# Optimization experiments

Measured on AMD Instinct MI355X. Metric: run time of the kernel, lower is better.

Reference implementation:

```python
import jax, jax.numpy as jnp
import numpy as np

B, S, D, H = 2, 2048, 1024, 16
HD = D // H            # head_dim = 64
CHUNK = 1024           # hard-coded in the torch module
ROPE_THETA = 10000.0


def setup_inputs() -> dict:
    key = jax.random.key(0)
    ks = jax.random.split(key, 5)
    hidden_states = jax.random.normal(ks[0], (B, S, D), dtype=jnp.float32)
    # Precomputed RoPE frequencies: freqs_cis[s, j] = exp(i * s * theta_j),
    # stored as real [S, HD//2, 2] = (cos, sin).
    inv_freq = 1.0 / (ROPE_THETA ** (np.arange(0, HD, 2, dtype=np.float32) / HD))
    ang = np.outer(np.arange(S, dtype=np.float32), inv_freq)  # [S, HD//2]
    freqs_cis = jnp.stack([jnp.cos(ang), jnp.sin(ang)], axis=-1).astype(jnp.float32)
    scale = 0.02
    Wq = jax.random.normal(ks[1], (D, D), dtype=jnp.float32) * scale
    Wk = jax.random.normal(ks[2], (D, D), dtype=jnp.float32) * scale
    Wv = jax.random.normal(ks[3], (D, D), dtype=jnp.float32) * scale
    Wo = jax.random.normal(ks[4], (D, D), dtype=jnp.float32) * scale
    return {"hidden_states": hidden_states, "freqs_cis": freqs_cis,
            "Wq": Wq, "Wk": Wk, "Wv": Wv, "Wo": Wo}


def _apply_rope(x, freqs_cis):
    # x: [B, S, H, HD]; freqs_cis: [S, HD//2, 2] (cos, sin)
    b, s, h, hd = x.shape
    xr = x.reshape(b, s, h, hd // 2, 2)
    a, bb = xr[..., 0], xr[..., 1]
    c = freqs_cis[:s, :, 0][None, :, None, :]  # broadcast over batch, heads
    d = freqs_cis[:s, :, 1][None, :, None, :]
    # complex multiply (a + ib)(c + id)
    out = jnp.stack([a * c - bb * d, a * d + bb * c], axis=-1)
    return out.reshape(b, s, h, hd)


def reference(hidden_states, freqs_cis, Wq, Wk, Wv, Wo):
    b, s, dm = hidden_states.shape
    q = (hidden_states @ Wq).reshape(b, s, H, HD)
    k = (hidden_states @ Wk).reshape(b, s, H, HD)
    v = (hidden_states @ Wv).reshape(b, s, H, HD)
    q = _apply_rope(q, freqs_cis)
    k = _apply_rope(k, freqs_cis)
    q = q.transpose(0, 2, 1, 3)  # [B, H, S, HD]
    k = k.transpose(0, 2, 1, 3)
    v = v.transpose(0, 2, 1, 3)
    scaling = HD ** (-0.5)
    out = jnp.zeros_like(q)
    # Faithful replication of the (buggy) chunked attention: softmax is
    # normalized PER key-chunk, then chunk outputs are summed.
    for i in range(0, s, CHUNK):
        j = min(i + CHUNK, s)
        w = jnp.einsum('bhqd,bhkd->bhqk', q, k[:, :, i:j]) * scaling
        w = jax.nn.softmax(w.astype(jnp.float32), axis=-1).astype(q.dtype)
        out = out + jnp.einsum('bhqk,bhkd->bhqd', w, v[:, :, i:j])
    out = out.transpose(0, 2, 1, 3).reshape(b, s, dm)
    return out @ Wo
```

## Files before the change

kernel.cpp:

```cpp
#include <hip/hip_runtime.h>
#include <hip/hip_bf16.h>
#include <cstdint>

typedef __bf16 bf16x8 __attribute__((ext_vector_type(8)));
typedef float f32x4 __attribute__((ext_vector_type(4)));
typedef float f32x16 __attribute__((ext_vector_type(16)));

#define MFMA16(a, b, c) __builtin_amdgcn_mfma_f32_16x16x32_bf16(a, b, c, 0, 0, 0)
#define MFMA32(a, b, c) __builtin_amdgcn_mfma_f32_32x32x16_bf16(a, b, c, 0, 0, 0)

__device__ __forceinline__ void gload_lds16(const void* g, void* l) {
  __builtin_amdgcn_global_load_lds(
      (const __attribute__((address_space(1))) unsigned int*)g,
      (__attribute__((address_space(3))) unsigned int*)l, 16, 0, 0);
}

__device__ __forceinline__ unsigned short f2bf(float x) {
  union { float f; uint32_t u; } v; v.f = x;
  uint32_t r = v.u + 0x7fff + ((v.u >> 16) & 1);
  return (unsigned short)(r >> 16);
}
__device__ __forceinline__ float bf2f(unsigned short h) {
  union { float f; uint32_t u; } v; v.u = ((uint32_t)h) << 16;
  return v.f;
}
__device__ __forceinline__ f32x16 fzero16() {
  f32x16 v;
#pragma unroll
  for (int i = 0; i < 16; ++i) v[i] = 0.f;
  return v;
}

__device__ __forceinline__ void ptrans(const f32x16& sv, float& rsum,
                                       bf16x8& f0, bf16x8& f1) {
  float ps[16];
#pragma unroll
  for (int r = 0; r < 16; ++r) ps[r] = __builtin_exp2f(sv[r]);
  float rs = 0.f;
#pragma unroll
  for (int r = 0; r < 16; ++r) rs += ps[r];
  rsum += rs;
  bf16x8 a, b;
#pragma unroll
  for (int r = 0; r < 8; ++r) a[r] = (__bf16)ps[r];
#pragma unroll
  for (int r = 0; r < 8; ++r) b[r] = (__bf16)ps[8 + r];
  f0 = a; f1 = b;
}

__global__ __launch_bounds__(256) void k_split(const float* __restrict__ x,
                                               unsigned short* __restrict__ hi, int n4) {
  int i = blockIdx.x * blockDim.x + threadIdx.x;
  if (i >= n4) return;
  float4 v = ((const float4*)x)[i];
  ushort4 h;
  h.x = f2bf(v.x); h.y = f2bf(v.y); h.z = f2bf(v.z); h.w = f2bf(v.w);
  ((ushort4*)hi)[i] = h;
}

__global__ __launch_bounds__(256) void k_wsplit(
    const float* __restrict__ Wq, const float* __restrict__ Wk,
    const float* __restrict__ Wv, const float* __restrict__ Wo,
    unsigned short* __restrict__ WtqH, unsigned short* __restrict__ WtkH,
    unsigned short* __restrict__ WtvH, unsigned short* __restrict__ WtoH) {
  const int z = blockIdx.z;
  const float* W = (z == 0) ? Wq : (z == 1) ? Wk : (z == 2) ? Wv : Wo;
  unsigned short* WtH = (z == 0) ? WtqH : (z == 1) ? WtkH : (z == 2) ? WtvH : WtoH;
  __shared__ float tile[32][33];
  const int bx = blockIdx.x, by = blockIdx.y;
  const int tx = threadIdx.x & 31, ty = threadIdx.x >> 5;
#pragma unroll
  for (int i = 0; i < 4; ++i)
    tile[ty + i * 8][tx] = W[(size_t)(by * 32 + ty + i * 8) * 1024 + bx * 32 + tx];
  __syncthreads();
#pragma unroll
  for (int i = 0; i < 4; ++i) {
    float v = tile[tx][ty + i * 8];
    WtH[(size_t)(bx * 32 + ty + i * 8) * 1024 + by * 32 + tx] = f2bf(v);
  }
}

__global__ __launch_bounds__(256, 2) void k_qkv(
    const unsigned short* __restrict__ hsH,
    const unsigned short* __restrict__ WqH, const unsigned short* __restrict__ WkH,
    const unsigned short* __restrict__ WvH, const float* __restrict__ freqs,
    unsigned short* __restrict__ qB, unsigned short* __restrict__ kB,
    unsigned short* __restrict__ vB) {
  __shared__ unsigned short Ah[128 * 32], Bh[128 * 32];
  const int tid = threadIdx.x;
  const int bm = blockIdx.y, bn = blockIdx.x;
  const int w = bn >> 3;
  const int n0 = (bn & 7) * 128;
  const unsigned short* WH = (w == 0) ? WqH : (w == 1) ? WkH : WvH;
  const int lane = tid & 63, wave = tid >> 6;
  const int wm = (wave & 1) * 64, wn = (wave >> 1) * 64;
  const int l15 = lane & 15, lq = lane >> 4;

  f32x4 acc[4][4];
#pragma unroll
  for (int i = 0; i < 4; i++)
#pragma unroll
    for (int j = 0; j < 4; j++) acc[i][j] = (f32x4){0.f, 0.f, 0.f, 0.f};

  const char* baseA = (const char*)hsH + (size_t)(bm * 128) * 2048;
  const char* baseB = (const char*)WH + (size_t)n0 * 2048;
  const int off0 = tid << 4, row0 = off0 >> 6, seg0 = off0 & 63;
  const int off1 = (tid + 256) << 4, row1 = off1 >> 6, seg1 = off1 & 63;

  for (int k0 = 0; k0 < 1024; k0 += 32) {
    __syncthreads();
    gload_lds16(baseA + (size_t)row0 * 2048 + k0 * 2 + seg0, (char*)Ah + wave * 1024);
    gload_lds16(baseB + (size_t)row0 * 2048 + k0 * 2 + seg0, (char*)Bh + wave * 1024);
    gload_lds16(baseA + (size_t)row1 * 2048 + k0 * 2 + seg1,
                (char*)Ah + 4096 + wave * 1024);
    gload_lds16(baseB + (size_t)row1 * 2048 + k0 * 2 + seg1,
                (char*)Bh + 4096 + wave * 1024);
    __syncthreads();
    bf16x8 ah[4], bh[4];
#pragma unroll
    for (int i = 0; i < 4; ++i) {
      ah[i] = *(const bf16x8*)&Ah[(wm + i * 16 + l15) * 32 + lq * 8];
      bh[i] = *(const bf16x8*)&Bh[(wn + i * 16 + l15) * 32 + lq * 8];
    }
#pragma unroll
    for (int i = 0; i < 4; ++i)
#pragma unroll
      for (int j = 0; j < 4; ++j) acc[i][j] = MFMA16(ah[i], bh[j], acc[i][j]);
  }

  unsigned short* dst = (w == 0) ? qB : (w == 1) ? kB : vB;
#pragma unroll
  for (int i = 0; i < 4; ++i) {
#pragma unroll
    for (int j = 0; j < 4; ++j) {
      int colw = n0 + wn + j * 16 + l15;
      int h = colw >> 6, d = colw & 63;
#pragma unroll
      for (int r = 0; r < 4; ++r) {
        int rowg = bm * 128 + wm + i * 16 + lq * 4 + r;
        int s = rowg & 2047, b = rowg >> 11;
        float val = acc[i][j][r];
        size_t bhb = (size_t)(b * 16 + h) * 131072;
        if (w < 2) {
          float partner = __shfl_xor(val, 1);
          int jj = d >> 1;
          float2 cssn = ((const float2*)freqs)[s * 32 + jj];
          float cs = cssn.x, sn = cssn.y;
          float res = (d & 1) ? (partner * sn + val * cs) : (val * cs - partner * sn);
          if (w == 0) {
            res *= 0.18033688011112042f;
            dst[(((size_t)(b * 16 + h)) * 2048 + s) * 64 + d] = f2bf(res);
          } else {
            size_t off = (size_t)(s >> 10) * 65536 + ((s >> 6) & 15) * 4096 +
                         ((s >> 5) & 1) * 2048 + (d >> 4) * 512 +
                         ((s & 31) + 32 * ((d >> 3) & 1)) * 8 + (d & 7);
            dst[bhb + off] = f2bf(res);
          }
        } else {
          int sp = (s & ~12) | ((s & 4) << 1) | ((s & 8) >> 1);
          size_t off = (size_t)(sp >> 10) * 65536 + ((sp >> 6) & 15) * 4096 +
                       (d >> 5) * 2048 + ((sp >> 4) & 3) * 512 +
                       ((d & 31) + 32 * ((sp >> 3) & 1)) * 8 + (sp & 7);
          dst[bhb + off] = f2bf(val);
        }
      }
    }
  }
}

__global__ __launch_bounds__(256, 4) void k_attn(
    const unsigned short* __restrict__ qB, const unsigned short* __restrict__ kB,
    const unsigned short* __restrict__ vB,
    unsigned short* __restrict__ c0, unsigned short* __restrict__ c1) {
  __shared__ unsigned short KV[2][8192];
  const int tid = threadIdx.x, lane = tid & 63, wave = tid >> 6;
  const int l31 = lane & 31, lh = lane >> 5;
  const int bid = blockIdx.x;
  const int x = (bid >> 3) & 15;
  const int gg = (bid & 7) + 8 * (bid >> 7);
  const int bh = gg & 31;
  const int chunk = gg >> 5;
  const int q0 = x * 128 + wave * 32;
  const size_t base = (size_t)bh * 131072;

  bf16x8 qf[4];
#pragma unroll
  for (int ks = 0; ks < 4; ++ks)
    qf[ks] = *(const bf16x8*)(qB + base + (size_t)(q0 + l31) * 64 + ks * 16 + lh * 8);

  const unsigned short* kblk = kB + base + chunk * 65536;
  const unsigned short* vblk = vB + base + chunk * 65536;

  gload_lds16((const char*)kblk + tid * 16, (char*)KV[0] + wave * 1024);
  gload_lds16((const char*)kblk + 4096 + tid * 16, (char*)KV[0] + 4096 + wave * 1024);
  gload_lds16((const char*)vblk + tid * 16, (char*)KV[0] + 8192 + wave * 1024);
  gload_lds16((const char*)vblk + 4096 + tid * 16, (char*)KV[0] + 12288 + wave * 1024);
  __syncthreads();

  f32x16 o[2];
#pragma unroll
  for (int a = 0; a < 2; ++a) o[a] = fzero16();
  float rsum = 0.f;

  for (int kb = 0; kb < 16; ++kb) {
    const unsigned short* Kc = KV[kb & 1];
    const unsigned short* Vc = KV[kb & 1] + 4096;
    if (kb < 15) {
      const char* ks_ = (const char*)(kblk + (kb + 1) * 4096);
      const char* vs_ = (const char*)(vblk + (kb + 1) * 4096);
      char* db = (char*)KV[(kb + 1) & 1];
      gload_lds16(ks_ + tid * 16, db + wave * 1024);
      gload_lds16(ks_ + 4096 + tid * 16, db + 4096 + wave * 1024);
      gload_lds16(vs_ + tid * 16, db + 8192 + wave * 1024);
      gload_lds16(vs_ + 4096 + tid * 16, db + 12288 + wave * 1024);
    }

    f32x16 sA = fzero16(), sB = fzero16();
    {
      bf16x8 kf[4];
#pragma unroll
      for (int ks = 0; ks < 4; ++ks)
        kf[ks] = *(const bf16x8*)(Kc + ks * 512 + lane * 8);
      __builtin_amdgcn_s_setprio(1);
#pragma unroll
      for (int ks = 0; ks < 4; ++ks) sA = MFMA32(kf[ks], qf[ks], sA);
      __builtin_amdgcn_s_setprio(0);
    }
    {
      bf16x8 kf[4];
#pragma unroll
      for (int ks = 0; ks < 4; ++ks)
        kf[ks] = *(const bf16x8*)(Kc + 2048 + ks * 512 + lane * 8);
      __builtin_amdgcn_s_setprio(1);
#pragma unroll
      for (int ks = 0; ks < 4; ++ks) sB = MFMA32(kf[ks], qf[ks], sB);
      __builtin_amdgcn_s_setprio(0);
    }

    bf16x8 vf[2][4];
#pragma unroll
    for (int dt = 0; dt < 2; ++dt)
#pragma unroll
      for (int ks = 0; ks < 4; ++ks)
        vf[dt][ks] = *(const bf16x8*)(Vc + dt * 2048 + ks * 512 + lane * 8);

    bf16x8 fA0, fA1, fB0, fB1;
    ptrans(sA, rsum, fA0, fA1);
    __builtin_amdgcn_s_setprio(1);
    o[0] = MFMA32(vf[0][0], fA0, o[0]);
    o[1] = MFMA32(vf[1][0], fA0, o[1]);
    o[0] = MFMA32(vf[0][1], fA1, o[0]);
    o[1] = MFMA32(vf[1][1], fA1, o[1]);
    __builtin_amdgcn_s_setprio(0);
    ptrans(sB, rsum, fB0, fB1);
    __builtin_amdgcn_s_setprio(1);
    o[0] = MFMA32(vf[0][2], fB0, o[0]);
    o[1] = MFMA32(vf[1][2], fB0, o[1]);
    o[0] = MFMA32(vf[0][3], fB1, o[0]);
    o[1] = MFMA32(vf[1][3], fB1, o[1]);
    __builtin_amdgcn_s_setprio(0);

    __syncthreads();
  }

  unsigned short* cB = chunk ? c1 : c0;
  const int b = bh >> 4, h = bh & 15;
  float lsum = rsum + __shfl_xor(rsum, 32);
  float inv = 1.f / lsum;
  int s = q0 + l31;
#pragma unroll
  for (int dt = 0; dt < 2; ++dt)
#pragma unroll
    for (int g = 0; g < 4; ++g) {
      int d = dt * 32 + 4 * lh + 8 * g;
      size_t idx = ((size_t)(b * 2048 + s)) * 1024 + h * 64 + d;
      ushort4 hv;
#pragma unroll
      for (int t = 0; t < 4; ++t)
        ((unsigned short*)&hv)[t] = f2bf(o[dt][g * 4 + t] * inv);
      *(ushort4*)(cB + idx) = hv;
    }
}

__global__ __launch_bounds__(256) void k_comb(const unsigned short* __restrict__ c0,
                                              const unsigned short* __restrict__ c1,
                                              unsigned short* __restrict__ outB,
                                              int n8) {
  int i = blockIdx.x * blockDim.x + threadIdx.x;
  if (i >= n8) return;
  uint4 a = ((const uint4*)c0)[i];
  uint4 b = ((const uint4*)c1)[i];
  uint4 r;
  const unsigned short* pa = (const unsigned short*)&a;
  const unsigned short* pb = (const unsigned short*)&b;
  unsigned short* pr = (unsigned short*)&r;
#pragma unroll
  for (int j = 0; j < 8; ++j) pr[j] = f2bf(bf2f(pa[j]) + bf2f(pb[j]));
  ((uint4*)outB)[i] = r;
}

__global__ __launch_bounds__(256, 2) void k_out(const unsigned short* __restrict__ A,
                                                const unsigned short* __restrict__ B,
                                                float* __restrict__ out) {
  __shared__ unsigned short Ah[128 * 32], Bh[64 * 32];
  const int tid = threadIdx.x;
  const int bm = blockIdx.y, n0 = blockIdx.x * 64;
  const int lane = tid & 63, wave = tid >> 6;
  const int wm = (wave & 1) * 64, wn = (wave >> 1) * 32;
  const int l15 = lane & 15, lq = lane >> 4;

  f32x4 acc[4][2];
#pragma unroll
  for (int i = 0; i < 4; i++)
#pragma unroll
    for (int j = 0; j < 2; j++) acc[i][j] = (f32x4){0.f, 0.f, 0.f, 0.f};

  const char* baseA = (const char*)A + (size_t)(bm * 128) * 2048;
  const char* baseB = (const char*)B + (size_t)n0 * 2048;
  const int off0 = tid << 4, row0 = off0 >> 6, seg0 = off0 & 63;
  const int off1 = (tid + 256) << 4, row1 = off1 >> 6, seg1 = off1 & 63;

  for (int k0 = 0; k0 < 1024; k0 += 32) {
    __syncthreads();
    gload_lds16(baseA + (size_t)row0 * 2048 + k0 * 2 + seg0, (char*)Ah + wave * 1024);
    gload_lds16(baseA + (size_t)row1 * 2048 + k0 * 2 + seg1,
                (char*)Ah + 4096 + wave * 1024);
    gload_lds16(baseB + (size_t)row0 * 2048 + k0 * 2 + seg0, (char*)Bh + wave * 1024);
    __syncthreads();
    bf16x8 ah[4], bh[2];
#pragma unroll
    for (int i = 0; i < 4; ++i)
      ah[i] = *(const bf16x8*)&Ah[(wm + i * 16 + l15) * 32 + lq * 8];
#pragma unroll
    for (int j = 0; j < 2; ++j)
      bh[j] = *(const bf16x8*)&Bh[(wn + j * 16 + l15) * 32 + lq * 8];
#pragma unroll
    for (int i = 0; i < 4; ++i)
#pragma unroll
      for (int j = 0; j < 2; ++j) acc[i][j] = MFMA16(ah[i], bh[j], acc[i][j]);
  }
#pragma unroll
  for (int i = 0; i < 4; ++i)
#pragma unroll
    for (int j = 0; j < 2; ++j) {
      int colw = n0 + wn + j * 16 + l15;
#pragma unroll
      for (int r = 0; r < 4; ++r) {
        int rowg = bm * 128 + wm + i * 16 + lq * 4 + r;
        out[(size_t)rowg * 1024 + colw] = acc[i][j][r];
      }
    }
}

extern "C" void kernel_launch(void* const* d_in, const int* in_sizes, int n_in,
                              void* d_out, int out_size, void* d_ws, size_t ws_size,
                              hipStream_t stream) {
  const float* hs = (const float*)d_in[0];
  const float* freqs = (const float*)d_in[1];
  const float* Wq = (const float*)d_in[2];
  const float* Wk = (const float*)d_in[3];
  const float* Wv = (const float*)d_in[4];
  const float* Wo = (const float*)d_in[5];
  float* out = (float*)d_out;

  const size_t MD = (size_t)4096 * 1024;
  const size_t WW = (size_t)1024 * 1024;
  unsigned short* hsH = (unsigned short*)d_ws;
  unsigned short* WtqH = hsH + MD;
  unsigned short* WtkH = WtqH + WW;
  unsigned short* WtvH = WtkH + WW;
  unsigned short* WtoH = WtvH + WW;
  unsigned short* qB = WtoH + WW;
  unsigned short* kB = qB + MD;
  unsigned short* vB = kB + MD;
  unsigned short* c0 = vB + MD;
  unsigned short* c1 = c0 + MD;
  unsigned short* attnB = hsH;

  k_split<<<4096, 256, 0, stream>>>(hs, hsH, (int)(MD / 4));
  k_wsplit<<<dim3(32, 32, 4), 256, 0, stream>>>(Wq, Wk, Wv, Wo,
                                                WtqH, WtkH, WtvH, WtoH);
  k_qkv<<<dim3(24, 32), 256, 0, stream>>>(hsH, WtqH, WtkH, WtvH, freqs, qB, kB, vB);
  k_attn<<<1024, 256, 0, stream>>>(qB, kB, vB, c0, c1);
  k_comb<<<2048, 256, 0, stream>>>(c0, c1, attnB, (int)(MD / 8));
  k_out<<<dim3(16, 32), 256, 0, stream>>>(attnB, WtoH, out);
}
```

Before: 213.2 us.

## Fuse hidden-state bf16 conversion into QKV GEMM and merge attention chunks

```diff
diff --git a/kernel.cpp b/kernel.cpp
--- a/kernel.cpp
+++ b/kernel.cpp
@@ -20,10 +20,6 @@
   uint32_t r = v.u + 0x7fff + ((v.u >> 16) & 1);
   return (unsigned short)(r >> 16);
 }
-__device__ __forceinline__ float bf2f(unsigned short h) {
-  union { float f; uint32_t u; } v; v.u = ((uint32_t)h) << 16;
-  return v.f;
-}
 __device__ __forceinline__ f32x16 fzero16() {
   f32x16 v;
 #pragma unroll
@@ -46,16 +42,6 @@
 #pragma unroll
   for (int r = 0; r < 8; ++r) b[r] = (__bf16)ps[8 + r];
   f0 = a; f1 = b;
-}
-
-__global__ __launch_bounds__(256) void k_split(const float* __restrict__ x,
-                                               unsigned short* __restrict__ hi, int n4) {
-  int i = blockIdx.x * blockDim.x + threadIdx.x;
-  if (i >= n4) return;
-  float4 v = ((const float4*)x)[i];
-  ushort4 h;
-  h.x = f2bf(v.x); h.y = f2bf(v.y); h.z = f2bf(v.z); h.w = f2bf(v.w);
-  ((ushort4*)hi)[i] = h;
 }
 
 __global__ __launch_bounds__(256) void k_wsplit(
@@ -81,12 +67,13 @@
 }
 
 __global__ __launch_bounds__(256, 2) void k_qkv(
-    const unsigned short* __restrict__ hsH,
+    const float* __restrict__ hs,
     const unsigned short* __restrict__ WqH, const unsigned short* __restrict__ WkH,
     const unsigned short* __restrict__ WvH, const float* __restrict__ freqs,
     unsigned short* __restrict__ qB, unsigned short* __restrict__ kB,
     unsigned short* __restrict__ vB) {
-  __shared__ unsigned short Ah[128 * 32], Bh[128 * 32];
+  __shared__ float Af[128 * 32];
+  __shared__ unsigned short Bh[128 * 32];
   const int tid = threadIdx.x;
   const int bm = blockIdx.y, bn = blockIdx.x;
   const int w = bn >> 3;
@@ -102,24 +89,38 @@
 #pragma unroll
     for (int j = 0; j < 4; j++) acc[i][j] = (f32x4){0.f, 0.f, 0.f, 0.f};
 
-  const char* baseA = (const char*)hsH + (size_t)(bm * 128) * 2048;
+  const char* baseA = (const char*)hs + (size_t)(bm * 128) * 4096;
   const char* baseB = (const char*)WH + (size_t)n0 * 2048;
-  const int off0 = tid << 4, row0 = off0 >> 6, seg0 = off0 & 63;
-  const int off1 = (tid + 256) << 4, row1 = off1 >> 6, seg1 = off1 & 63;
+  const int off0 = tid << 4, brow0 = off0 >> 6, bseg0 = off0 & 63;
+  const int off1 = (tid + 256) << 4, brow1 = off1 >> 6, bseg1 = off1 & 63;
 
   for (int k0 = 0; k0 < 1024; k0 += 32) {
     __syncthreads();
-    gload_lds16(baseA + (size_t)row0 * 2048 + k0 * 2 + seg0, (char*)Ah + wave * 1024);
-    gload_lds16(baseB + (size_t)row0 * 2048 + k0 * 2 + seg0, (char*)Bh + wave * 1024);
-    gload_lds16(baseA + (size_t)row1 * 2048 + k0 * 2 + seg1,
-                (char*)Ah + 4096 + wave * 1024);
-    gload_lds16(baseB + (size_t)row1 * 2048 + k0 * 2 + seg1,
+#pragma unroll
+    for (int g = 0; g < 4; ++g) {
+      int offa = g * 4096 + tid * 16;
+      int arow = offa >> 7, aseg = offa & 127;
+      gload_lds16(baseA + (size_t)arow * 4096 + k0 * 4 + aseg,
+                  (char*)Af + g * 4096 + wave * 1024);
+    }
+    gload_lds16(baseB + (size_t)brow0 * 2048 + k0 * 2 + bseg0,
+                (char*)Bh + wave * 1024);
+    gload_lds16(baseB + (size_t)brow1 * 2048 + k0 * 2 + bseg1,
                 (char*)Bh + 4096 + wave * 1024);
     __syncthreads();
     bf16x8 ah[4], bh[4];
 #pragma unroll
     for (int i = 0; i < 4; ++i) {
-      ah[i] = *(const bf16x8*)&Ah[(wm + i * 16 + l15) * 32 + lq * 8];
+      int ar = wm + i * 16 + l15;
+      f32x4 a0 = *(const f32x4*)&Af[ar * 32 + lq * 8];
+      f32x4 a1 = *(const f32x4*)&Af[ar * 32 + lq * 8 + 4];
+      bf16x8 v;
+#pragma unroll
+      for (int j = 0; j < 4; ++j) {
+        v[j] = (__bf16)a0[j];
+        v[4 + j] = (__bf16)a1[j];
+      }
+      ah[i] = v;
       bh[i] = *(const bf16x8*)&Bh[(wn + i * 16 + l15) * 32 + lq * 8];
     }
 #pragma unroll
@@ -168,18 +169,70 @@
   }
 }
 
-__global__ __launch_bounds__(256, 4) void k_attn(
+#define ATTN_KB(KB, OAC, RS, PREF)                                            \
+  {                                                                           \
+    const unsigned short* Kc = KV[(KB) & 1];                                  \
+    const unsigned short* Vc = KV[(KB) & 1] + 4096;                           \
+    if (PREF) {                                                               \
+      const char* ks_ = (const char*)(kblk + ((KB) + 1) * 4096);              \
+      const char* vs_ = (const char*)(vblk + ((KB) + 1) * 4096);              \
+      char* db = (char*)KV[((KB) + 1) & 1];                                   \
+      gload_lds16(ks_ + tid * 16, db + wave * 1024);                          \
+      gload_lds16(ks_ + 4096 + tid * 16, db + 4096 + wave * 1024);            \
+      gload_lds16(vs_ + tid * 16, db + 8192 + wave * 1024);                   \
+      gload_lds16(vs_ + 4096 + tid * 16, db + 12288 + wave * 1024);           \
+    }                                                                         \
+    f32x16 sA = fzero16(), sB = fzero16();                                    \
+    {                                                                         \
+      bf16x8 kf[4];                                                           \
+      _Pragma("unroll") for (int ks = 0; ks < 4; ++ks)                        \
+          kf[ks] = *(const bf16x8*)(Kc + ks * 512 + lane * 8);                \
+      __builtin_amdgcn_s_setprio(1);                                          \
+      _Pragma("unroll") for (int ks = 0; ks < 4; ++ks)                        \
+          sA = MFMA32(kf[ks], qf[ks], sA);                                    \
+      __builtin_amdgcn_s_setprio(0);                                          \
+    }                                                                         \
+    {                                                                         \
+      bf16x8 kf[4];                                                           \
+      _Pragma("unroll") for (int ks = 0; ks < 4; ++ks)                        \
+          kf[ks] = *(const bf16x8*)(Kc + 2048 + ks * 512 + lane * 8);         \
+      __builtin_amdgcn_s_setprio(1);                                          \
+      _Pragma("unroll") for (int ks = 0; ks < 4; ++ks)                        \
+          sB = MFMA32(kf[ks], qf[ks], sB);                                    \
+      __builtin_amdgcn_s_setprio(0);                                          \
+    }                                                                         \
+    bf16x8 vf[2][4];                                                          \
+    _Pragma("unroll") for (int dt = 0; dt < 2; ++dt)                          \
+        _Pragma("unroll") for (int ks = 0; ks < 4; ++ks)                      \
+            vf[dt][ks] = *(const bf16x8*)(Vc + dt * 2048 + ks * 512 +         \
+                                          lane * 8);                          \
+    bf16x8 fA0, fA1, fB0, fB1;                                                \
+    ptrans(sA, RS, fA0, fA1);                                                 \
+    __builtin_amdgcn_s_setprio(1);                                            \
+    OAC[0] = MFMA32(vf[0][0], fA0, OAC[0]);                                   \
+    OAC[1] = MFMA32(vf[1][0], fA0, OAC[1]);                                   \
+    OAC[0] = MFMA32(vf[0][1], fA1, OAC[0]);                                   \
+    OAC[1] = MFMA32(vf[1][1], fA1, OAC[1]);                                   \
+    __builtin_amdgcn_s_setprio(0);                                            \
+    ptrans(sB, RS, fB0, fB1);                                                 \
+    __builtin_amdgcn_s_setprio(1);                                            \
+    OAC[0] = MFMA32(vf[0][2], fB0, OAC[0]);                                   \
+    OAC[1] = MFMA32(vf[1][2], fB0, OAC[1]);                                   \
+    OAC[0] = MFMA32(vf[0][3], fB1, OAC[0]);                                   \
+    OAC[1] = MFMA32(vf[1][3], fB1, OAC[1]);                                   \
+    __builtin_amdgcn_s_setprio(0);                                            \
+    __syncthreads();                                                          \
+  }
+
+__global__ __launch_bounds__(256, 2) void k_attn(
     const unsigned short* __restrict__ qB, const unsigned short* __restrict__ kB,
-    const unsigned short* __restrict__ vB,
-    unsigned short* __restrict__ c0, unsigned short* __restrict__ c1) {
+    const unsigned short* __restrict__ vB, unsigned short* __restrict__ outB) {
   __shared__ unsigned short KV[2][8192];
   const int tid = threadIdx.x, lane = tid & 63, wave = tid >> 6;
   const int l31 = lane & 31, lh = lane >> 5;
   const int bid = blockIdx.x;
   const int x = (bid >> 3) & 15;
-  const int gg = (bid & 7) + 8 * (bid >> 7);
-  const int bh = gg & 31;
-  const int chunk = gg >> 5;
+  const int bh = (bid & 7) + 8 * (bid >> 7);
   const int q0 = x * 128 + wave * 32;
   const size_t base = (size_t)bh * 131072;
 
@@ -188,8 +241,8 @@
   for (int ks = 0; ks < 4; ++ks)
     qf[ks] = *(const bf16x8*)(qB + base + (size_t)(q0 + l31) * 64 + ks * 16 + lh * 8);
 
-  const unsigned short* kblk = kB + base + chunk * 65536;
-  const unsigned short* vblk = vB + base + chunk * 65536;
+  const unsigned short* kblk = kB + base;
+  const unsigned short* vblk = vB + base;
 
   gload_lds16((const char*)kblk + tid * 16, (char*)KV[0] + wave * 1024);
   gload_lds16((const char*)kblk + 4096 + tid * 16, (char*)KV[0] + 4096 + wave * 1024);
@@ -197,76 +250,18 @@
   gload_lds16((const char*)vblk + 4096 + tid * 16, (char*)KV[0] + 12288 + wave * 1024);
   __syncthreads();
 
-  f32x16 o[2];
-#pragma unroll
-  for (int a = 0; a < 2; ++a) o[a] = fzero16();
-  float rsum = 0.f;
-
-  for (int kb = 0; kb < 16; ++kb) {
-    const unsigned short* Kc = KV[kb & 1];
-    const unsigned short* Vc = KV[kb & 1] + 4096;
-    if (kb < 15) {
-      const char* ks_ = (const char*)(kblk + (kb + 1) * 4096);
-      const char* vs_ = (const char*)(vblk + (kb + 1) * 4096);
-      char* db = (char*)KV[(kb + 1) & 1];
-      gload_lds16(ks_ + tid * 16, db + wave * 1024);
-      gload_lds16(ks_ + 4096 + tid * 16, db + 4096 + wave * 1024);
-      gload_lds16(vs_ + tid * 16, db + 8192 + wave * 1024);
-      gload_lds16(vs_ + 4096 + tid * 16, db + 12288 + wave * 1024);
-    }
-
-    f32x16 sA = fzero16(), sB = fzero16();
-    {
-      bf16x8 kf[4];
-#pragma unroll
-      for (int ks = 0; ks < 4; ++ks)
-        kf[ks] = *(const bf16x8*)(Kc + ks * 512 + lane * 8);
-      __builtin_amdgcn_s_setprio(1);
-#pragma unroll
-      for (int ks = 0; ks < 4; ++ks) sA = MFMA32(kf[ks], qf[ks], sA);
-      __builtin_amdgcn_s_setprio(0);
-    }
-    {
-      bf16x8 kf[4];
-#pragma unroll
-      for (int ks = 0; ks < 4; ++ks)
-        kf[ks] = *(const bf16x8*)(Kc + 2048 + ks * 512 + lane * 8);
-      __builtin_amdgcn_s_setprio(1);
-#pragma unroll
-      for (int ks = 0; ks < 4; ++ks) sB = MFMA32(kf[ks], qf[ks], sB);
-      __builtin_amdgcn_s_setprio(0);
-    }
-
-    bf16x8 vf[2][4];
-#pragma unroll
-    for (int dt = 0; dt < 2; ++dt)
-#pragma unroll
-      for (int ks = 0; ks < 4; ++ks)
-        vf[dt][ks] = *(const bf16x8*)(Vc + dt * 2048 + ks * 512 + lane * 8);
-
-    bf16x8 fA0, fA1, fB0, fB1;
-    ptrans(sA, rsum, fA0, fA1);
-    __builtin_amdgcn_s_setprio(1);
-    o[0] = MFMA32(vf[0][0], fA0, o[0]);
-    o[1] = MFMA32(vf[1][0], fA0, o[1]);
-    o[0] = MFMA32(vf[0][1], fA1, o[0]);
-    o[1] = MFMA32(vf[1][1], fA1, o[1]);
-    __builtin_amdgcn_s_setprio(0);
-    ptrans(sB, rsum, fB0, fB1);
-    __builtin_amdgcn_s_setprio(1);
-    o[0] = MFMA32(vf[0][2], fB0, o[0]);
-    o[1] = MFMA32(vf[1][2], fB0, o[1]);
-    o[0] = MFMA32(vf[0][3], fB1, o[0]);
-    o[1] = MFMA32(vf[1][3], fB1, o[1]);
-    __builtin_amdgcn_s_setprio(0);
-
-    __syncthreads();
-  }
-
-  unsigned short* cB = chunk ? c1 : c0;
+  f32x16 o0[2], o1[2];
+#pragma unroll
+  for (int a = 0; a < 2; ++a) { o0[a] = fzero16(); o1[a] = fzero16(); }
+  float rs0 = 0.f, rs1 = 0.f;
+
+  for (int kb = 0; kb < 16; ++kb) ATTN_KB(kb, o0, rs0, 1)
+  for (int kb = 16; kb < 32; ++kb) ATTN_KB(kb, o1, rs1, (kb < 31))
+
   const int b = bh >> 4, h = bh & 15;
-  float lsum = rsum + __shfl_xor(rsum, 32);
-  float inv = 1.f / lsum;
+  float l0 = rs0 + __shfl_xor(rs0, 32);
+  float l1 = rs1 + __shfl_xor(rs1, 32);
+  float inv0 = 1.f / l0, inv1 = 1.f / l1;
   int s = q0 + l31;
 #pragma unroll
   for (int dt = 0; dt < 2; ++dt)
@@ -277,26 +272,10 @@
       ushort4 hv;
 #pragma unroll
       for (int t = 0; t < 4; ++t)
-        ((unsigned short*)&hv)[t] = f2bf(o[dt][g * 4 + t] * inv);
-      *(ushort4*)(cB + idx) = hv;
-    }
-}
-
-__global__ __launch_bounds__(256) void k_comb(const unsigned short* __restrict__ c0,
-                                              const unsigned short* __restrict__ c1,
-                                              unsigned short* __restrict__ outB,
-                                              int n8) {
-  int i = blockIdx.x * blockDim.x + threadIdx.x;
-  if (i >= n8) return;
-  uint4 a = ((const uint4*)c0)[i];
-  uint4 b = ((const uint4*)c1)[i];
-  uint4 r;
-  const unsigned short* pa = (const unsigned short*)&a;
-  const unsigned short* pb = (const unsigned short*)&b;
-  unsigned short* pr = (unsigned short*)&r;
-#pragma unroll
-  for (int j = 0; j < 8; ++j) pr[j] = f2bf(bf2f(pa[j]) + bf2f(pb[j]));
-  ((uint4*)outB)[i] = r;
+        ((unsigned short*)&hv)[t] =
+            f2bf(o0[dt][g * 4 + t] * inv0 + o1[dt][g * 4 + t] * inv1);
+      *(ushort4*)(outB + idx) = hv;
+    }
 }
 
 __global__ __launch_bounds__(256, 2) void k_out(const unsigned short* __restrict__ A,
@@ -365,23 +344,18 @@
 
   const size_t MD = (size_t)4096 * 1024;
   const size_t WW = (size_t)1024 * 1024;
-  unsigned short* hsH = (unsigned short*)d_ws;
-  unsigned short* WtqH = hsH + MD;
+  unsigned short* WtqH = (unsigned short*)d_ws;
   unsigned short* WtkH = WtqH + WW;
   unsigned short* WtvH = WtkH + WW;
   unsigned short* WtoH = WtvH + WW;
   unsigned short* qB = WtoH + WW;
   unsigned short* kB = qB + MD;
   unsigned short* vB = kB + MD;
-  unsigned short* c0 = vB + MD;
-  unsigned short* c1 = c0 + MD;
-  unsigned short* attnB = hsH;
-
-  k_split<<<4096, 256, 0, stream>>>(hs, hsH, (int)(MD / 4));
+  unsigned short* attnB = vB + MD;
+
   k_wsplit<<<dim3(32, 32, 4), 256, 0, stream>>>(Wq, Wk, Wv, Wo,
                                                 WtqH, WtkH, WtvH, WtoH);
-  k_qkv<<<dim3(24, 32), 256, 0, stream>>>(hsH, WtqH, WtkH, WtvH, freqs, qB, kB, vB);
-  k_attn<<<1024, 256, 0, stream>>>(qB, kB, vB, c0, c1);
-  k_comb<<<2048, 256, 0, stream>>>(c0, c1, attnB, (int)(MD / 8));
+  k_qkv<<<dim3(24, 32), 256, 0, stream>>>(hs, WtqH, WtkH, WtvH, freqs, qB, kB, vB);
+  k_attn<<<512, 256, 0, stream>>>(qB, kB, vB, attnB);
   k_out<<<dim3(16, 32), 256, 0, stream>>>(attnB, WtoH, out);
 }
```

After: 212.5 us. Within noise of the previous version (-0.3%).
